# Kernel tuning notes

Measured on AMD Instinct MI355X. Metric: run time of the kernel, lower is better.

The kernel has to match this reference:

```python
import jax, jax.numpy as jnp
import numpy as np

# t2t / fold constants (FuseFormer defaults)
K = 7      # kernel size
S = 3      # stride
P = 3      # padding
H, W = 60, 108          # fold output_size
LH = (H + 2 * P - K) // S + 1   # 20
LW = (W + 2 * P - K) // S + 1   # 36
NVECS = LH * LW                 # 720


def _patch_indices():
    # row[k, i] = k + S*i : row coordinate in the padded image for kernel offset k, window i
    row = jnp.arange(K)[:, None] + S * jnp.arange(LH)[None, :]   # [K, LH]
    col = jnp.arange(K)[:, None] + S * jnp.arange(LW)[None, :]   # [K, LW]
    R = row[:, None, :, None]   # [K,1,LH,1]
    C = col[None, :, None, :]   # [1,K,1,LW] -> broadcast [K,K,LH,LW]
    return R, C


def setup_inputs() -> dict:
    key = jax.random.key(0)
    ks = jax.random.split(key, 5)
    b, n, d, hd = 2, 5760, 512, 1960
    return {
        "x": jax.random.normal(ks[0], (b, n, d), dtype=jnp.float32),
        "W1": jax.random.normal(ks[1], (d, hd), dtype=jnp.float32) * 0.02,
        "b1": jax.random.normal(ks[2], (hd,), dtype=jnp.float32) * 0.02,
        "W2": jax.random.normal(ks[3], (hd, d), dtype=jnp.float32) * 0.02,
        "b2": jax.random.normal(ks[4], (d,), dtype=jnp.float32) * 0.02,
    }


def reference(x, W1, b1, W2, b2):
    b, n, d = x.shape
    h = x @ W1 + b1                      # [b, n, 1960]
    c = h.shape[-1]
    Cch = c // (K * K)                   # 40 channels
    B2 = (b * n) // NVECS                # folded batch

    R, Cc = _patch_indices()

    # fold(x): [B2, C*K*K, L] scatter-add (col2im) into padded image
    hf = h.reshape(B2, NVECS, c).transpose(0, 2, 1)            # [B2, c, L]
    hf = hf.reshape(B2, Cch, K, K, LH, LW)
    padded = jnp.zeros((B2, Cch, H + 2 * P, W + 2 * P), h.dtype)
    padded = padded.at[:, :, R, Cc].add(hf)
    folded = padded[:, :, P:P + H, P:P + W]                    # [B2, C, H, W]

    # fold(ones): overlap-count normalizer (batch-independent, compute once)
    ones6 = jnp.ones((1, 1, K, K, LH, LW), h.dtype)
    npad = jnp.zeros((1, 1, H + 2 * P, W + 2 * P), h.dtype)
    norm = npad.at[:, :, R, Cc].add(ones6)[:, :, P:P + H, P:P + W]

    y = folded / norm                                          # broadcast over channels

    # unfold: im2col gather of 7x7 patches
    ypad = jnp.pad(y, ((0, 0), (0, 0), (P, P), (P, P)))
    patches = ypad[:, :, R, Cc]                                # [B2, C, K, K, LH, LW]
    uf = patches.reshape(B2, c, NVECS).transpose(0, 2, 1).reshape(b, n, c)

    # conv2: ReLU -> (dropout=identity at eval) -> Linear -> (dropout)
    out = jnp.maximum(uf, 0) @ W2 + b2                         # [b, n, d]
    return out
```

## Files before the change

kernel.cpp:

```cpp
#include <hip/hip_runtime.h>
#include <hip/hip_bf16.h>

#define M_ROWS   11520
#define D_IN     512
#define HD       1960
#define HDP      2048
#define CPAD     52
#define K2       2080
#define B2C      16
#define NVECS    720
#define LH       20
#define LW       36
#define HH       60
#define WW       108
#define CCH      40

using bf16x8 = __attribute__((ext_vector_type(8))) short;
using f32x4  = __attribute__((ext_vector_type(4))) float;
using f4     = __attribute__((ext_vector_type(4))) float;
using su4    = __attribute__((ext_vector_type(4))) unsigned short;

__device__ __forceinline__ float bf2f(unsigned short u) {
    unsigned int x = ((unsigned int)u) << 16;
    return __builtin_bit_cast(float, x);
}
__device__ __forceinline__ unsigned short f2bf(float f) {
    unsigned int x = __builtin_bit_cast(unsigned int, f);
    unsigned int r = (x + 0x7fffu + ((x >> 16) & 1u)) >> 16;
    return (unsigned short)r;
}

__device__ __forceinline__ void gl_lds16(const unsigned short* g, unsigned short* l) {
    __builtin_amdgcn_global_load_lds(
        (const __attribute__((address_space(1))) unsigned int*)g,
        (__attribute__((address_space(3))) unsigned int*)l, 16, 0, 0);
}

__global__ __launch_bounds__(256) void prep(
    const float* __restrict__ x, const float* __restrict__ W1, const float* __restrict__ W2,
    unsigned short* __restrict__ xb, unsigned short* __restrict__ w1t,
    unsigned short* __restrict__ w2t)
{
    __shared__ unsigned short tile[32][33];
    int b = blockIdx.x, t = threadIdx.x;
    if (b < 5760) {
        int i = b * 256 + t;
        f4 v = ((const f4*)x)[i];
        su4 o;
        o.x = f2bf(v.x); o.y = f2bf(v.y); o.z = f2bf(v.z); o.w = f2bf(v.w);
        ((su4*)xb)[i] = o;
        return;
    }
    int tx = t & 31, ty = t >> 5;
    if (b < 6784) {
        int blk = b - 5760;
        int kt = blk & 15, nt = blk >> 4;
        int k0 = kt * 32, n0 = nt * 32;
#pragma unroll
        for (int p = 0; p < 4; p++) {
            int k = k0 + ty + p * 8;
            int n = n0 + tx;
            tile[ty + p * 8][tx] = (n < HD) ? f2bf(W1[k * HD + n]) : (unsigned short)0;
        }
        __syncthreads();
#pragma unroll
        for (int p = 0; p < 4; p++) {
            int n = n0 + ty + p * 8;
            int k = k0 + tx;
            w1t[n * 512 + k] = tile[tx][ty + p * 8];
        }
    } else {
        int blk = b - 6784;
        int kt = blk % 62, nt = blk / 62;
        int k0 = kt * 32, n0 = nt * 32;
#pragma unroll
        for (int p = 0; p < 4; p++) {
            int k = k0 + ty + p * 8;
            int n = n0 + tx;
            tile[ty + p * 8][tx] = (k < HD) ? f2bf(W2[k * 512 + n]) : (unsigned short)0;
        }
        __syncthreads();
#pragma unroll
        for (int p = 0; p < 4; p++) {
            int n = n0 + ty + p * 8;
            int k = k0 + tx;
            if (k < HD) {
                int cch = k / 49, kk = k - cch * 49;
                w2t[n * K2 + cch * CPAD + kk] = tile[tx][ty + p * 8];
            }
        }
    }
}

__global__ __launch_bounds__(256) void gemm1_blk(
    const unsigned short* __restrict__ A,
    const unsigned short* __restrict__ Bt,
    const float* __restrict__ bias,
    unsigned short* __restrict__ h_blk)
{
    __shared__ unsigned short sA[2 * 128 * 32];
    __shared__ unsigned short sB[2 * 128 * 32];
    const int lda = D_IN, ldb = D_IN;
    const int NT = D_IN / 32;

    int g = (blockIdx.x & 7) * 180 + (blockIdx.x >> 3);
    int bx = g & 15, by = g >> 4;
    int t    = threadIdx.x;
    int w    = t >> 6;
    int lane = t & 63;
    int quad = lane >> 4;
    int l16  = lane & 15;
    int row0 = by * 128, col0 = bx * 128;
    int wr = (w >> 1) * 64, wc = (w & 1) * 64;

    int srow = t >> 2;
    int qb = ((t & 3) - ((srow >> 1) & 3)) & 3;
    const unsigned short* Ag = A  + (size_t)(row0 + srow) * lda + qb * 8;
    const unsigned short* Bg = Bt + (size_t)(col0 + srow) * ldb + qb * 8;
    unsigned short* lA = sA + t * 8;
    unsigned short* lB = sB + t * 8;

    int xq = (quad + ((l16 >> 1) & 3)) & 3;

    f32x4 acc[4][4] = {};

    gl_lds16(Ag, lA);
    gl_lds16(Ag + (size_t)64 * lda, lA + 2048);
    gl_lds16(Bg, lB);
    gl_lds16(Bg + (size_t)64 * ldb, lB + 2048);
    __syncthreads();

    for (int it = 0; it < NT; ++it) {
        int cur = it & 1, nxt = cur ^ 1;
        if (it + 1 < NT) {
            int k0n = (it + 1) * 32;
            gl_lds16(Ag + k0n, lA + nxt * 4096);
            gl_lds16(Ag + (size_t)64 * lda + k0n, lA + nxt * 4096 + 2048);
            gl_lds16(Bg + k0n, lB + nxt * 4096);
            gl_lds16(Bg + (size_t)64 * ldb + k0n, lB + nxt * 4096 + 2048);
        }
        const unsigned short* bA = sA + cur * 4096;
        const unsigned short* bB = sB + cur * 4096;

        bf16x8 a[4], bfr[4];
#pragma unroll
        for (int i = 0; i < 4; i++)
            a[i] = *(const bf16x8*)(bA + (wr + i * 16 + l16) * 32 + xq * 8);
#pragma unroll
        for (int j = 0; j < 4; j++)
            bfr[j] = *(const bf16x8*)(bB + (wc + j * 16 + l16) * 32 + xq * 8);
#pragma unroll
        for (int i = 0; i < 4; i++)
#pragma unroll
            for (int j = 0; j < 4; j++)
                acc[i][j] = __builtin_amdgcn_mfma_f32_16x16x32_bf16(a[i], bfr[j], acc[i][j], 0, 0, 0);
        __syncthreads();
    }

    int rowterm[16];
#pragma unroll
    for (int i = 0; i < 4; i++)
#pragma unroll
        for (int r = 0; r < 4; r++) {
            int row = row0 + wr + i * 16 + quad * 4 + r;
            int bb = row / NVECS;
            int sp = row - bb * NVECS;
            rowterm[i * 4 + r] = bb * (CCH * NVECS * CPAD) + sp * CPAD;
        }

#pragma unroll
    for (int j = 0; j < 4; j++) {
        int col = col0 + wc + j * 16 + l16;
        if (col < HD) {
            int cch = col / 49, kk = col - cch * 49;
            int colterm = cch * (NVECS * CPAD) + kk;
            float bv = bias[col];
#pragma unroll
            for (int i = 0; i < 4; i++)
#pragma unroll
                for (int r = 0; r < 4; r++)
                    h_blk[(size_t)rowterm[i * 4 + r] + colterm] = f2bf(acc[i][j][r] + bv);
        }
    }
}

__global__ __launch_bounds__(256) void fold_unfold(
    const unsigned short* __restrict__ h_blk,
    unsigned short* __restrict__ uf)
{
    __shared__ unsigned short h_lds[12 * 36 * CPAD];
    __shared__ unsigned short y_lds[33 * WW];
    int bid  = blockIdx.x;
    int half = bid & 1;
    int cch  = (bid >> 1) % CCH;
    int b2   = bid / (CCH * 2);
    int tid  = threadIdx.x;

    int lh_base = half ? 8 : 0;
    int y0 = half ? 27 : 0;
    int ny = half ? 33 : 31;

    const su4* hsrc = (const su4*)(h_blk +
        ((size_t)(b2 * CCH + cch) * NVECS + lh_base * 36) * CPAD);
    su4* hd = (su4*)h_lds;
    for (int i = tid; i < 12 * 36 * CPAD / 4; i += 256)
        hd[i] = hsrc[i];
    __syncthreads();

    for (int idx = tid; idx < ny * WW; idx += 256) {
        int rr = idx / WW, c = idx - rr * WW;
        int r  = y0 + rr;
        int rp = r + 3, cp = c + 3;
        int q1 = rp / 3, rem1 = rp - q1 * 3;
        int q2 = cp / 3, rem2 = cp - q2 * 3;
        bool rv0 = (q1 <= 19);
        bool rv2 = (rem1 == 0) & (q1 >= 2);
        int sl0 = q1 - lh_base, sl1 = sl0 - 1, sl2 = sl0 - 2;
        int rofs0 = rem1 * 7, rofs1 = rofs0 + 21, rofs2 = rofs0 + 42;
        bool cv0 = (q2 <= 35);
        bool cv2 = (rem2 == 0) & (q2 >= 2);
        int lw0 = q2, lw1 = q2 - 1, lw2 = q2 - 2;
        int n1 = 1 + (int)rv0 + (int)rv2;
        int n2 = 1 + (int)cv0 + (int)cv2;
        float s = 0.0f;
#define FTERM(vr, sl, rofs, vc, lw, cofs) {                                   \
        bool vv = (vr) & (vc);                                                \
        int ad = vv ? (((sl) * 36 + (lw)) * CPAD + (rofs) + (cofs)) : 0;      \
        float val = bf2f(h_lds[ad]);                                          \
        s += vv ? val : 0.0f; }
        FTERM(rv0,  sl0, rofs0, cv0,  lw0, rem2)
        FTERM(rv0,  sl0, rofs0, true, lw1, rem2 + 3)
        FTERM(rv0,  sl0, rofs0, cv2,  lw2, rem2 + 6)
        FTERM(true, sl1, rofs1, cv0,  lw0, rem2)
        FTERM(true, sl1, rofs1, true, lw1, rem2 + 3)
        FTERM(true, sl1, rofs1, cv2,  lw2, rem2 + 6)
        FTERM(rv2,  sl2, rofs2, cv0,  lw0, rem2)
        FTERM(rv2,  sl2, rofs2, true, lw1, rem2 + 3)
        FTERM(rv2,  sl2, rofs2, cv2,  lw2, rem2 + 6)
#undef FTERM
        y_lds[idx] = f2bf(fmaxf(s / (float)(n1 * n2), 0.0f));
    }
    __syncthreads();

    int lh0 = 10 * half;
    for (int i = tid; i < 360 * 13; i += 256) {
        int ri = i / 13, q = i - ri * 13;
        int lh = lh0 + ri / 36;
        int lw = ri % 36;
        int rb = 3 * lh - 3, cb = 3 * lw - 3;
        int j0 = q * 4;
        su4 o;
#pragma unroll
        for (int e = 0; e < 4; e++) {
            int j = j0 + e;
            unsigned short val = 0;
            if (j < 49) {
                int k1 = j / 7, k2 = j - k1 * 7;
                int r = rb + k1, cc = cb + k2;
                if ((unsigned)r < (unsigned)HH && (unsigned)cc < (unsigned)WW)
                    val = y_lds[(r - y0) * WW + cc];
            }
            ((unsigned short*)&o)[e] = val;
        }
        int row = b2 * NVECS + lh * 36 + lw;
        *(su4*)(uf + (size_t)row * K2 + cch * CPAD + j0) = o;
    }
}

__global__ __launch_bounds__(256) void gemm2(
    const unsigned short* __restrict__ A,
    const unsigned short* __restrict__ Bt,
    const float* __restrict__ bias,
    float* __restrict__ C)
{
    __shared__ unsigned short sA[2 * 128 * 32];
    __shared__ unsigned short sB[2 * 64 * 32];
    const int lda = K2, ldb = K2, ldc = D_IN;
    const int NT = K2 / 32;

    int g = (blockIdx.x & 7) * 90 + (blockIdx.x >> 3);
    int bx = g & 7, by = g >> 3;
    int t    = threadIdx.x;
    int w    = t >> 6;
    int lane = t & 63;
    int quad = lane >> 4;
    int l16  = lane & 15;
    int row0 = by * 128, col0 = bx * 64;
    int wr = (w >> 1) * 64, wc = (w & 1) * 32;

    int srow = t >> 2;
    int qb = ((t & 3) - ((srow >> 1) & 3)) & 3;
    const unsigned short* Ag = A  + (size_t)(row0 + srow) * lda + qb * 8;
    const unsigned short* Bg = Bt + (size_t)(col0 + srow) * ldb + qb * 8;
    unsigned short* lA = sA + t * 8;
    unsigned short* lB = sB + t * 8;

    int xq = (quad + ((l16 >> 1) & 3)) & 3;

    f32x4 acc[4][2] = {};

    gl_lds16(Ag, lA);
    gl_lds16(Ag + (size_t)64 * lda, lA + 2048);
    gl_lds16(Bg, lB);
    __syncthreads();

    for (int it = 0; it < NT; ++it) {
        int cur = it & 1, nxt = cur ^ 1;
        if (it + 1 < NT) {
            int k0n = (it + 1) * 32;
            gl_lds16(Ag + k0n, lA + nxt * 4096);
            gl_lds16(Ag + (size_t)64 * lda + k0n, lA + nxt * 4096 + 2048);
            gl_lds16(Bg + k0n, lB + nxt * 2048);
        }
        const unsigned short* bA = sA + cur * 4096;
        const unsigned short* bB = sB + cur * 2048;

        bf16x8 a[4], bfr[2];
#pragma unroll
        for (int i = 0; i < 4; i++)
            a[i] = *(const bf16x8*)(bA + (wr + i * 16 + l16) * 32 + xq * 8);
#pragma unroll
        for (int j = 0; j < 2; j++)
            bfr[j] = *(const bf16x8*)(bB + (wc + j * 16 + l16) * 32 + xq * 8);
#pragma unroll
        for (int i = 0; i < 4; i++)
#pragma unroll
            for (int j = 0; j < 2; j++)
                acc[i][j] = __builtin_amdgcn_mfma_f32_16x16x32_bf16(a[i], bfr[j], acc[i][j], 0, 0, 0);
        __syncthreads();
    }

#pragma unroll
    for (int j = 0; j < 2; j++) {
        int col = col0 + wc + j * 16 + l16;
        float bv = bias[col];
#pragma unroll
        for (int i = 0; i < 4; i++) {
            int rbase = row0 + wr + i * 16 + quad * 4;
#pragma unroll
            for (int r = 0; r < 4; r++)
                C[(size_t)(rbase + r) * ldc + col] = acc[i][j][r] + bv;
        }
    }
}

extern "C" void kernel_launch(void* const* d_in, const int* in_sizes, int n_in,
                              void* d_out, int out_size, void* d_ws, size_t ws_size,
                              hipStream_t stream) {
    const float* x   = (const float*)d_in[0];
    const float* W1  = (const float*)d_in[1];
    const float* b1  = (const float*)d_in[2];
    const float* W2  = (const float*)d_in[3];
    const float* b2f = (const float*)d_in[4];
    float* out = (float*)d_out;

    unsigned short* ws    = (unsigned short*)d_ws;
    unsigned short* xb    = ws;
    unsigned short* h_blk = xb + (size_t)M_ROWS * D_IN;
    unsigned short* uf    = h_blk + (size_t)M_ROWS * K2;
    unsigned short* w1t   = uf + (size_t)M_ROWS * K2;
    unsigned short* w2t   = w1t + (size_t)HDP * D_IN;

    hipLaunchKernelGGL(prep, dim3(7776), dim3(256), 0, stream, x, W1, W2, xb, w1t, w2t);

    hipLaunchKernelGGL(gemm1_blk, dim3((M_ROWS / 128) * (HDP / 128)), dim3(256), 0, stream,
                       xb, w1t, b1, h_blk);

    hipLaunchKernelGGL(fold_unfold, dim3(B2C * CCH * 2), dim3(256), 0, stream, h_blk, uf);

    hipLaunchKernelGGL(gemm2, dim3((M_ROWS / 128) * (D_IN / 64)), dim3(256), 0, stream,
                       uf, w2t, b2f, out);
}
```

Before: 220.5 us.

## Overlap prefetch with compute using partial vmcnt waits; zero pad columns in-kernel

Both GEMM main loops now wait only for the current K-tile's global-to-LDS loads (s_waitcnt vmcnt(N)) before a raw barrier, instead of a full __syncthreads that drained all outstanding loads, including the next tile's prefetch. This lets the prefetch stay in flight while the MFMAs run. The pad columns of the h_blk and w2t buffers (channel slots 49-51) are also zeroed by the producing kernels, likely so the workspace no longer needs a separate memset. The hand-written waitcnt counts depend on the compiler not reordering or merging the LDS-direct loads, which risks correctness.

```diff
diff --git a/kernel.cpp b/kernel.cpp
--- a/kernel.cpp
+++ b/kernel.cpp
@@ -73,6 +73,13 @@
         int blk = b - 6784;
         int kt = blk % 62, nt = blk / 62;
         int k0 = kt * 32, n0 = nt * 32;
+        if (kt == 0) {
+            for (int i = t; i < 32 * CCH * 3; i += 256) {
+                int nn = n0 + (i & 31);
+                int cc = (i >> 5) / 3, p = (i >> 5) % 3;
+                w2t[nn * K2 + cc * CPAD + 49 + p] = 0;
+            }
+        }
 #pragma unroll
         for (int p = 0; p < 4; p++) {
             int k = k0 + ty + p * 8;
@@ -128,7 +135,6 @@
     gl_lds16(Ag + (size_t)64 * lda, lA + 2048);
     gl_lds16(Bg, lB);
     gl_lds16(Bg + (size_t)64 * ldb, lB + 2048);
-    __syncthreads();
 
     for (int it = 0; it < NT; ++it) {
         int cur = it & 1, nxt = cur ^ 1;
@@ -138,7 +144,13 @@
             gl_lds16(Ag + (size_t)64 * lda + k0n, lA + nxt * 4096 + 2048);
             gl_lds16(Bg + k0n, lB + nxt * 4096);
             gl_lds16(Bg + (size_t)64 * ldb + k0n, lB + nxt * 4096 + 2048);
-        }
+            asm volatile("s_waitcnt vmcnt(4)" ::: "memory");
+        } else {
+            asm volatile("s_waitcnt vmcnt(0)" ::: "memory");
+        }
+        __builtin_amdgcn_s_barrier();
+        asm volatile("" ::: "memory");
+
         const unsigned short* bA = sA + cur * 4096;
         const unsigned short* bB = sB + cur * 4096;
 
@@ -154,7 +166,9 @@
 #pragma unroll
             for (int j = 0; j < 4; j++)
                 acc[i][j] = __builtin_amdgcn_mfma_f32_16x16x32_bf16(a[i], bfr[j], acc[i][j], 0, 0, 0);
-        __syncthreads();
+        asm volatile("" ::: "memory");
+        __builtin_amdgcn_s_barrier();
+        asm volatile("" ::: "memory");
     }
 
     int rowterm[16];
@@ -181,6 +195,19 @@
                 for (int r = 0; r < 4; r++)
                     h_blk[(size_t)rowterm[i * 4 + r] + colterm] = f2bf(acc[i][j][r] + bv);
         }
+    }
+
+    int cch0 = col0 / 49;
+    int cch1 = (col0 + 127) / 49; if (cch1 > CCH - 1) cch1 = CCH - 1;
+    int ncch = cch1 - cch0 + 1;
+    if (wc == 0 && l16 < 3 * ncch) {
+        int c = l16 / 3, p = l16 - c * 3;
+        int padcol = (cch0 + c) * (NVECS * CPAD) + 49 + p;
+#pragma unroll
+        for (int i = 0; i < 4; i++)
+#pragma unroll
+            for (int r = 0; r < 4; r++)
+                h_blk[(size_t)rowterm[i * 4 + r] + padcol] = 0;
     }
 }
 
@@ -302,7 +329,6 @@
     gl_lds16(Ag, lA);
     gl_lds16(Ag + (size_t)64 * lda, lA + 2048);
     gl_lds16(Bg, lB);
-    __syncthreads();
 
     for (int it = 0; it < NT; ++it) {
         int cur = it & 1, nxt = cur ^ 1;
@@ -311,7 +337,13 @@
             gl_lds16(Ag + k0n, lA + nxt * 4096);
             gl_lds16(Ag + (size_t)64 * lda + k0n, lA + nxt * 4096 + 2048);
             gl_lds16(Bg + k0n, lB + nxt * 2048);
-        }
+            asm volatile("s_waitcnt vmcnt(3)" ::: "memory");
+        } else {
+            asm volatile("s_waitcnt vmcnt(0)" ::: "memory");
+        }
+        __builtin_amdgcn_s_barrier();
+        asm volatile("" ::: "memory");
+
         const unsigned short* bA = sA + cur * 4096;
         const unsigned short* bB = sB + cur * 2048;
 
@@ -327,7 +359,9 @@
 #pragma unroll
             for (int j = 0; j < 2; j++)
                 acc[i][j] = __builtin_amdgcn_mfma_f32_16x16x32_bf16(a[i], bfr[j], acc[i][j], 0, 0, 0);
-        __syncthreads();
+        asm volatile("" ::: "memory");
+        __builtin_amdgcn_s_barrier();
+        asm volatile("" ::: "memory");
     }
 
 #pragma unroll
```

Result: no change. 221.0 us (+0.2%).
